# Kernel optimization log

Hardware: AMD Instinct MI355X
Metric: run time of the kernel (lower is better)

The kernel has to match this reference:

```python
import jax, jax.numpy as jnp
import numpy as np

B, S, D, H = 2, 2048, 1024, 16
HD = D // H  # head dim = 64


def setup_inputs() -> dict:
    key = jax.random.key(0)
    ks = jax.random.split(key, 9)
    s_in = 1.0 / np.sqrt(D)
    s_out = 1.0 / np.sqrt(HD)
    return {
        "x": jax.random.normal(ks[0], (B, S, D), jnp.float32),
        "Wq": jax.random.normal(ks[1], (D, H, HD), jnp.float32) * s_in,
        "bq": jnp.zeros((H, HD), jnp.float32),
        "Wk": jax.random.normal(ks[2], (D, H, HD), jnp.float32) * s_in,
        "bk": jnp.zeros((H, HD), jnp.float32),
        "Wv": jax.random.normal(ks[3], (D, H, HD), jnp.float32) * s_in,
        "bv": jnp.zeros((H, HD), jnp.float32),
        "Wo": jax.random.normal(ks[4], (H, HD, D), jnp.float32) * s_out,
        "bo": jnp.zeros((D,), jnp.float32),
    }


def reference(x, Wq, bq, Wk, bk, Wv, bv, Wo, bo):
    # QKV projections: [B,S,D] -> [B,S,H,HD]
    q = jnp.einsum("bsd,dhk->bshk", x, Wq) + bq
    k = jnp.einsum("bsd,dhk->bshk", x, Wk) + bk
    v = jnp.einsum("bsd,dhk->bshk", x, Wv) + bv

    # scaled dot-product attention (matches nnx.dot_product_attention)
    scale = jnp.asarray(1.0 / np.sqrt(HD), q.dtype)
    scores = jnp.einsum("bqhk,bshk->bhqs", q * scale, k)  # [B,H,S,S]
    attn = jax.nn.softmax(scores, axis=-1)
    y = jnp.einsum("bhqs,bshk->bqhk", attn, v)  # [B,S,H,HD]

    # exclusive post-processing: subtract projection onto L2-normalized v
    eps = jnp.asarray(1e-12, v.dtype)
    v_norm = v * jax.lax.rsqrt(jnp.sum(jnp.square(v), axis=-1, keepdims=True) + eps)
    y = y - jnp.sum(y * v_norm, axis=-1, keepdims=True) * v_norm

    # output projection: [B,S,H,HD] -> [B,S,D]
    out = jnp.einsum("bshk,hkd->bsd", y, Wo) + bo
    return out  # dropout is identity (deterministic=True)
```

## Files before the change

kernel.cpp:

```cpp
#include <hip/hip_runtime.h>

#define BB 2
#define SS 2048
#define DD 1024
#define HH 16
#define HDD 64

typedef __attribute__((ext_vector_type(4))) float f32x4;
typedef __attribute__((ext_vector_type(8))) short short8;
typedef __attribute__((ext_vector_type(4))) short short4v;

__device__ __forceinline__ short f2bf(float f) {
    union { float f; unsigned u; } a; a.f = f;
    unsigned r = a.u + 0x7fffu + ((a.u >> 16) & 1u);
    return (short)(r >> 16);
}
__device__ __forceinline__ float bf2f(short s) {
    union { unsigned u; float f; } a; a.u = ((unsigned)(unsigned short)s) << 16;
    return a.f;
}
__device__ __forceinline__ float fast_exp2(float x) {
    float r;
    asm("v_exp_f32 %0, %1\n\ts_nop 0" : "=v"(r) : "v"(x));
    return r;
}
__device__ __forceinline__ unsigned cvt_pk_bf16(float lo, float hi) {
    unsigned r;
    asm("v_cvt_pk_bf16_f32 %0, %1, %2" : "=v"(r) : "v"(lo), "v"(hi));
    return r;
}
__device__ __forceinline__ float fmax3(float a, float b, float c) {
    float r;
    asm("v_max3_f32 %0, %1, %2, %3" : "=v"(r) : "v"(a), "v"(b), "v"(c));
    return r;
}

#define GLD16(gp, lp) __builtin_amdgcn_global_load_lds( \
    (const __attribute__((address_space(1))) void*)(gp), \
    (__attribute__((address_space(3))) void*)(lp), 16, 0, 0)

__global__ __launch_bounds__(256) void conv_all(
    const float* __restrict__ x,
    const float* __restrict__ Wq, const float* __restrict__ Wk,
    const float* __restrict__ Wv, const float* __restrict__ Wo,
    short* __restrict__ xb, short* __restrict__ Wt, short* __restrict__ Wot,
    float qscale)
{
    const int z = blockIdx.z;
    if (z == 4) {
        const int id = blockIdx.x * 16 + blockIdx.y;
        const size_t base = (size_t)id * 16384 + threadIdx.x * 8;
        #pragma unroll
        for (int it = 0; it < 8; ++it) {
            const size_t i = base + (size_t)it * 2048;
            f32x4 a = *(const f32x4*)(x + i);
            f32x4 b = *(const f32x4*)(x + i + 4);
            short8 o;
            #pragma unroll
            for (int j = 0; j < 4; j++) { o[j] = f2bf(a[j]); o[j + 4] = f2bf(b[j]); }
            *(short8*)(xb + i) = o;
        }
        return;
    }
    __shared__ float t[64][65];
    const float* src = (z == 0) ? Wq : (z == 1) ? Wk : (z == 2) ? Wv : Wo;
    short* dst = (z < 3) ? (Wt + (size_t)z * 1048576) : Wot;
    const float scale = (z == 0) ? qscale : 1.f;

    const int tid = threadIdx.x;
    const int c = tid & 63, rg = tid >> 6;
    const int bi = blockIdx.x * 64, bj = blockIdx.y * 64;
    #pragma unroll
    for (int i = 0; i < 16; i++)
        t[rg * 16 + i][c] = src[(size_t)(bi + rg * 16 + i) * 1024 + bj + c];
    __syncthreads();
    #pragma unroll
    for (int i = 0; i < 16; i++)
        dst[(size_t)(bj + rg * 16 + i) * 1024 + bi + c] = f2bf(scale * t[c][rg * 16 + i]);
}

template<int KIND>
__global__ __launch_bounds__(256, 2) void gemm_mfma(
    const short* __restrict__ A, const short* __restrict__ Bt,
    const float* __restrict__ b0, const float* __restrict__ b1,
    const float* __restrict__ b2, float qscale,
    short* __restrict__ oQ, short* __restrict__ oK, short* __restrict__ oV,
    float* __restrict__ oF)
{
    __shared__ short lds[32768];
    const int tid = threadIdx.x;
    const int lane = tid & 63;
    const int ln15 = lane & 15, g = lane >> 4;
    const int swl = ln15 & 7;
    const int wid = tid >> 6;
    const int wm = wid >> 1, wn = wid & 1;
    const int bm = blockIdx.x * 128;
    const int bn = blockIdx.y * 128;
    const bool vpath = (KIND == 0) && (blockIdx.y >= 16);

    f32x4 acc[4][4];
    #pragma unroll
    for (int i = 0; i < 4; i++)
        #pragma unroll
        for (int j = 0; j < 4; j++) acc[i][j] = (f32x4){0.f, 0.f, 0.f, 0.f};

    const int sr = lane >> 3, cs = lane & 7;
    const int sc8 = (cs ^ sr) << 3;
    const int rb = wid * 8;
    const short* Ak = A;
    const short* Bk = Bt;
    int aoff[4], boff[4], adst[4];
    #pragma unroll
    for (int j = 0; j < 4; j++) {
        aoff[j] = (bm + rb + j * 32 + sr) * 1024 + sc8;
        boff[j] = (bn + rb + j * 32 + sr) * 1024 + sc8;
        adst[j] = (rb + j * 32) * 64;
    }

    auto stage = [&](int BUF) {
        #pragma unroll
        for (int j = 0; j < 4; j++) {
            GLD16(Ak + aoff[j], &lds[BUF * 16384 + adst[j]]);
            GLD16(Bk + boff[j], &lds[BUF * 16384 + 8192 + adst[j]]);
        }
        Ak += 64; Bk += 64;
    };

    const char* ldsc = (const char*)lds;
    int aB[2], bB[2];
    #pragma unroll
    for (int kk = 0; kk < 2; kk++) {
        aB[kk] = (wm * 64 + ln15) * 128 + ((((kk << 2) | g) ^ swl) << 4);
        bB[kk] = 16384 + (wn * 64 + ln15) * 128 + ((((kk << 2) | g) ^ swl) << 4);
    }

    auto tilec = [&](int BUF) {
        #pragma unroll
        for (int kk = 0; kk < 2; kk++) {
            short8 af[4], bf[4];
            #pragma unroll
            for (int f = 0; f < 4; f++) {
                af[f] = *(const short8*)(ldsc + BUF * 32768 + aB[kk] + f * 2048);
                bf[f] = *(const short8*)(ldsc + BUF * 32768 + bB[kk] + f * 2048);
            }
            if (!vpath) {
                #pragma unroll
                for (int fm = 0; fm < 4; fm++)
                    #pragma unroll
                    for (int fn = 0; fn < 4; fn++)
                        acc[fm][fn] = __builtin_amdgcn_mfma_f32_16x16x32_bf16(
                            bf[fn], af[fm], acc[fm][fn], 0, 0, 0);
            } else {
                #pragma unroll
                for (int fm = 0; fm < 4; fm++)
                    #pragma unroll
                    for (int fn = 0; fn < 4; fn++)
                        acc[fm][fn] = __builtin_amdgcn_mfma_f32_16x16x32_bf16(
                            af[fm], bf[fn], acc[fm][fn], 0, 0, 0);
            }
        }
    };

    stage(0);
    asm volatile("s_waitcnt vmcnt(0)" ::: "memory");
    __builtin_amdgcn_s_barrier();

    #pragma unroll 1
    for (int i = 0; i < 7; ++i) {
        stage(1);
        tilec(0);
        asm volatile("s_waitcnt vmcnt(0) lgkmcnt(0)" ::: "memory");
        __builtin_amdgcn_s_barrier();
        stage(0);
        tilec(1);
        asm volatile("s_waitcnt vmcnt(0) lgkmcnt(0)" ::: "memory");
        __builtin_amdgcn_s_barrier();
    }
    stage(1);
    tilec(0);
    asm volatile("s_waitcnt vmcnt(0) lgkmcnt(0)" ::: "memory");
    __builtin_amdgcn_s_barrier();
    tilec(1);

    const int n_base = bn + wn * 64;

    if constexpr (KIND == 1) {
        #pragma unroll
        for (int fn = 0; fn < 4; fn++) {
            const int n0 = n_base + fn * 16 + 4 * g;
            const f32x4 b4 = *(const f32x4*)(b0 + n0);
            #pragma unroll
            for (int fm = 0; fm < 4; fm++) {
                const int t = bm + wm * 64 + fm * 16 + ln15;
                f32x4 o = acc[fm][fn] + b4;
                *(f32x4*)(oF + (size_t)t * 1024 + n0) = o;
            }
        }
    } else if (!vpath) {
        const bool isq = (n_base < 1024);
        short* dst = isq ? oQ : oK;
        const float* bp = isq ? b0 : b1;
        const float scl = isq ? qscale : 1.f;
        #pragma unroll
        for (int fn = 0; fn < 4; fn++) {
            const int n0 = n_base + fn * 16 + 4 * g;
            const int nl = n0 & 1023;
            f32x4 b4 = *(const f32x4*)(bp + nl);
            b4 *= scl;
            const int h = nl >> 6, d = nl & 63;
            #pragma unroll
            for (int fm = 0; fm < 4; fm++) {
                const int t = bm + wm * 64 + fm * 16 + ln15;
                const int b = t >> 11, s = t & 2047;
                short4v pk = { f2bf(acc[fm][fn][0] + b4[0]), f2bf(acc[fm][fn][1] + b4[1]),
                               f2bf(acc[fm][fn][2] + b4[2]), f2bf(acc[fm][fn][3] + b4[3]) };
                *(short4v*)(dst + ((size_t)(b * HH + h) * SS + s) * HDD + d) = pk;
            }
        }
    } else {
        #pragma unroll
        for (int fn = 0; fn < 4; fn++) {
            const int nf = n_base + fn * 16 + ln15;
            const int nl = nf - 2048;
            const float bb = b2[nl];
            const int h = nl >> 6, d = nl & 63;
            #pragma unroll
            for (int fm = 0; fm < 4; fm++) {
                const int t0 = bm + wm * 64 + fm * 16 + 4 * g;
                const int b = t0 >> 11;
                const int sb = (t0 & 2047) & ~63;
                const int pos = g * 16 + (fm & 1) * 4 + ((fm >> 1) & 1) * 8;
                short4v pk = { f2bf(acc[fm][fn][0] + bb), f2bf(acc[fm][fn][1] + bb),
                               f2bf(acc[fm][fn][2] + bb), f2bf(acc[fm][fn][3] + bb) };
                *(short4v*)(oV + ((size_t)(b * HH + h) * HDD + d) * SS + sb + pos) = pk;
            }
        }
    }
}

__global__ __launch_bounds__(256, 2) void attn_mfma_kernel(
    const short* __restrict__ Qh, const short* __restrict__ Kh,
    const short* __restrict__ Vt, short* __restrict__ yb)
{
    __shared__ short lds[16384];

    const int lane = threadIdx.x & 63;
    const int wid  = threadIdx.x >> 6;
    const int ln15 = lane & 15;
    const int g    = lane >> 4;
    const int swl  = ln15 & 7;

    const int bid  = ((int)blockIdx.x & 7) * 64 + ((int)blockIdx.x >> 3);
    const int bh   = bid >> 4;
    const int qB   = (bid & 15) * 128;
    const int qW   = qB + wid * 32;

    const short* qbase = Qh + (size_t)bh * SS * HDD;
    const short* kbase = Kh + (size_t)bh * SS * HDD;
    const short* vtb   = Vt + (size_t)bh * HDD * SS;

    short8 qf[2][2];
    #pragma unroll
    for (int qg = 0; qg < 2; qg++)
        #pragma unroll
        for (int c = 0; c < 2; c++)
            qf[qg][c] = *(const short8*)(qbase +
                (size_t)(qW + qg * 16 + ln15) * HDD + c * 32 + g * 8);

    const short8 ones = { 0x3f80, 0x3f80, 0x3f80, 0x3f80,
                          0x3f80, 0x3f80, 0x3f80, 0x3f80 };

    const int sr = lane >> 3;
    const int cs = lane & 7;
    const int sc8 = (cs ^ sr) << 3;
    const int r0 = wid * 16 + sr;
    const int r1 = wid * 16 + 8 + sr;
    const short* Kk = kbase;
    const short* Vk = vtb;
    const int koff0 = r0 * 64 + sc8, koff1 = r1 * 64 + sc8;
    const int voff0 = r0 * 2048 + sc8, voff1 = r1 * 2048 + sc8;
    const int d0 = (wid * 16) * 64, d1 = (wid * 16 + 8) * 64;

    auto stage = [&](int BUF) {
        GLD16(Kk + koff0, &lds[BUF * 8192 + d0]);
        GLD16(Kk + koff1, &lds[BUF * 8192 + d1]);
        GLD16(Vk + voff0, &lds[BUF * 8192 + 4096 + d0]);
        GLD16(Vk + voff1, &lds[BUF * 8192 + 4096 + d1]);
        Kk += 4096; Vk += 64;
    };

    const char* ldsc = (const char*)lds;
    const int kA0 = ln15 * 128 + ((g ^ swl) << 4);
    const int kA1 = ln15 * 128 + (((4 + g) ^ swl) << 4);
    const int vA0 = 8192 + ln15 * 128 + (((2 * g) ^ swl) << 4);
    const int vA1 = 8192 + ln15 * 128 + (((2 * g + 1) ^ swl) << 4);

    f32x4 o[2][4], ol[2];
    #pragma unroll
    for (int qg = 0; qg < 2; qg++) {
        ol[qg] = (f32x4){0.f, 0.f, 0.f, 0.f};
        #pragma unroll
        for (int c = 0; c < 4; c++) o[qg][c] = (f32x4){0.f, 0.f, 0.f, 0.f};
    }
    float m[2] = { -1e30f, -1e30f };

    auto tilec = [&](int BUF) {
        short8 kf[4][2];
        #pragma unroll
        for (int kg = 0; kg < 4; kg++) {
            kf[kg][0] = *(const short8*)(ldsc + BUF * 16384 + kA0 + kg * 2048);
            kf[kg][1] = *(const short8*)(ldsc + BUF * 16384 + kA1 + kg * 2048);
        }
        const f32x4 z = {0.f, 0.f, 0.f, 0.f};
        f32x4 s[4][2];
        __builtin_amdgcn_s_setprio(1);
        #pragma unroll
        for (int kg = 0; kg < 4; kg++)
            #pragma unroll
            for (int qg = 0; qg < 2; qg++) {
                s[kg][qg] = __builtin_amdgcn_mfma_f32_16x16x32_bf16(
                    kf[kg][0], qf[qg][0], z, 0, 0, 0);
                s[kg][qg] = __builtin_amdgcn_mfma_f32_16x16x32_bf16(
                    kf[kg][1], qf[qg][1], s[kg][qg], 0, 0, 0);
            }
        __builtin_amdgcn_s_setprio(0);

        float pm[2];
        #pragma unroll
        for (int qg = 0; qg < 2; qg++) {
            const float t0 = fmax3(s[0][qg][0], s[0][qg][1], s[0][qg][2]);
            const float t1 = fmax3(s[0][qg][3], s[1][qg][0], s[1][qg][1]);
            const float t2 = fmax3(s[1][qg][2], s[1][qg][3], s[2][qg][0]);
            const float t3 = fmax3(s[2][qg][1], s[2][qg][2], s[2][qg][3]);
            const float t4 = fmax3(s[3][qg][0], s[3][qg][1], s[3][qg][2]);
            pm[qg] = fmaxf(fmax3(t0, t1, t2), fmax3(t3, t4, s[3][qg][3]));
        }
        if (__any((pm[0] > m[0] + 8.f) || (pm[1] > m[1] + 8.f))) {
            #pragma unroll
            for (int qg = 0; qg < 2; qg++) {
                float pmw = fmaxf(pm[qg], __shfl_xor(pm[qg], 16));
                pmw = fmaxf(pmw, __shfl_xor(pmw, 32));
                const float mn = fmaxf(m[qg], pmw);
                const float corr = fast_exp2(m[qg] - mn);
                ol[qg] *= corr;
                #pragma unroll
                for (int c = 0; c < 4; c++) o[qg][c] *= corr;
                m[qg] = mn;
            }
        }

        union { unsigned u[4]; short8 v; } P0[2], P1[2];
        #pragma unroll
        for (int qg = 0; qg < 2; qg++) {
            float p[16];
            #pragma unroll
            for (int kg = 0; kg < 4; kg++)
                #pragma unroll
                for (int r = 0; r < 4; r++)
                    p[kg * 4 + r] = fast_exp2(s[kg][qg][r] - m[qg]);
            P0[qg].u[0] = cvt_pk_bf16(p[0], p[1]);
            P0[qg].u[1] = cvt_pk_bf16(p[2], p[3]);
            P0[qg].u[2] = cvt_pk_bf16(p[4], p[5]);
            P0[qg].u[3] = cvt_pk_bf16(p[6], p[7]);
            P1[qg].u[0] = cvt_pk_bf16(p[8], p[9]);
            P1[qg].u[1] = cvt_pk_bf16(p[10], p[11]);
            P1[qg].u[2] = cvt_pk_bf16(p[12], p[13]);
            P1[qg].u[3] = cvt_pk_bf16(p[14], p[15]);
        }

        __builtin_amdgcn_s_setprio(1);
        #pragma unroll
        for (int c = 0; c < 4; c++) {
            short8 vf0 = *(const short8*)(ldsc + BUF * 16384 + vA0 + c * 2048);
            short8 vf1 = *(const short8*)(ldsc + BUF * 16384 + vA1 + c * 2048);
            #pragma unroll
            for (int qg = 0; qg < 2; qg++) {
                o[qg][c] = __builtin_amdgcn_mfma_f32_16x16x32_bf16(
                    vf0, P0[qg].v, o[qg][c], 0, 0, 0);
                o[qg][c] = __builtin_amdgcn_mfma_f32_16x16x32_bf16(
                    vf1, P1[qg].v, o[qg][c], 0, 0, 0);
            }
        }
        #pragma unroll
        for (int qg = 0; qg < 2; qg++) {
            ol[qg] = __builtin_amdgcn_mfma_f32_16x16x32_bf16(ones, P0[qg].v, ol[qg], 0, 0, 0);
            ol[qg] = __builtin_amdgcn_mfma_f32_16x16x32_bf16(ones, P1[qg].v, ol[qg], 0, 0, 0);
        }
        __builtin_amdgcn_s_setprio(0);
    };

    stage(0);
    asm volatile("s_waitcnt vmcnt(0)" ::: "memory");
    __builtin_amdgcn_s_barrier();

    #pragma unroll 1
    for (int i = 0; i < 15; ++i) {
        stage(1);
        tilec(0);
        asm volatile("s_waitcnt vmcnt(0) lgkmcnt(0)" ::: "memory");
        __builtin_amdgcn_s_barrier();
        stage(0);
        tilec(1);
        asm volatile("s_waitcnt vmcnt(0) lgkmcnt(0)" ::: "memory");
        __builtin_amdgcn_s_barrier();
    }
    stage(1);
    tilec(0);
    asm volatile("s_waitcnt vmcnt(0) lgkmcnt(0)" ::: "memory");
    __builtin_amdgcn_s_barrier();
    tilec(1);

    const int b = bh >> 4, h = bh & 15;
    #pragma unroll
    for (int qg = 0; qg < 2; qg++) {
        const float inv = 1.f / ol[qg][0];
        #pragma unroll
        for (int c = 0; c < 4; c++) o[qg][c] *= inv;

        const int spos = qB + (wid >> 1) * 64 + (ln15 >> 2) * 16 + qg * 4 +
                         (wid & 1) * 8 + (ln15 & 3);
        float v4[4][4];
        float nv = 0.f, dv = 0.f;
        #pragma unroll
        for (int c = 0; c < 4; c++)
            #pragma unroll
            for (int r = 0; r < 4; r++) {
                const float vd = bf2f(vtb[(size_t)(c * 16 + 4 * g + r) * SS + spos]);
                v4[c][r] = vd;
                nv += vd * vd;
                dv += o[qg][c][r] * vd;
            }
        nv += __shfl_xor(nv, 16); nv += __shfl_xor(nv, 32);
        dv += __shfl_xor(dv, 16); dv += __shfl_xor(dv, 32);
        const float tpp = dv / (nv + 1e-12f);

        const int tok = b * SS + qW + qg * 16 + ln15;
        #pragma unroll
        for (int c = 0; c < 4; c++) {
            short4v pk = { f2bf(o[qg][c][0] - v4[c][0] * tpp),
                           f2bf(o[qg][c][1] - v4[c][1] * tpp),
                           f2bf(o[qg][c][2] - v4[c][2] * tpp),
                           f2bf(o[qg][c][3] - v4[c][3] * tpp) };
            *(short4v*)(yb + (size_t)tok * 1024 + h * 64 + c * 16 + 4 * g) = pk;
        }
    }
}

extern "C" void kernel_launch(void* const* d_in, const int* in_sizes, int n_in,
                              void* d_out, int out_size, void* d_ws, size_t ws_size,
                              hipStream_t stream)
{
    const float* x  = (const float*)d_in[0];
    const float* Wq = (const float*)d_in[1];
    const float* bq = (const float*)d_in[2];
    const float* Wk = (const float*)d_in[3];
    const float* bk = (const float*)d_in[4];
    const float* Wv = (const float*)d_in[5];
    const float* bv = (const float*)d_in[6];
    const float* Wo = (const float*)d_in[7];
    const float* bo = (const float*)d_in[8];
    float* out = (float*)d_out;

    char* w = (char*)d_ws;
    short* xb   = (short*)(w);
    short* Wt   = (short*)(w + (8ull << 20));
    short* Wot  = (short*)(w + (14ull << 20));
    short* Qh   = (short*)(w + (16ull << 20));
    short* Kh   = (short*)(w + (24ull << 20));
    short* Vt   = (short*)(w + (32ull << 20));
    short* yb   = (short*)(w + (40ull << 20));

    const float qscale = 0.125f * 1.44269504f;
    dim3 blk(256);

    conv_all<<<dim3(16, 16, 5), blk, 0, stream>>>(x, Wq, Wk, Wv, Wo,
                                                  xb, Wt, Wot, qscale);

    gemm_mfma<0><<<dim3(32, 24), blk, 0, stream>>>(xb, Wt, bq, bk, bv, qscale,
                                                   Qh, Kh, Vt, nullptr);

    attn_mfma_kernel<<<dim3(512), blk, 0, stream>>>(Qh, Kh, Vt, yb);

    gemm_mfma<1><<<dim3(32, 8), blk, 0, stream>>>(yb, Wot, bo, nullptr, nullptr, 1.f,
                                                  nullptr, nullptr, nullptr, out);
}
```

Before: 103.7 us.

## Double attention KV tile to 128 keys and shrink output-projection GEMM M tile

The attention kernel now stages 128 keys per step instead of 64, with a new swizzled V-transpose layout and twice the MFMAs per tile. This halves the number of loop iterations, barriers and online-softmax rescale checks. The output-projection GEMM uses 64-row M tiles and launches 512 blocks instead of 256, giving better CU occupancy on the small GEMM. The costs are doubled attention LDS use and higher register pressure from the larger score arrays, which may hurt occupancy.

```diff
diff --git a/kernel.cpp b/kernel.cpp
--- a/kernel.cpp
+++ b/kernel.cpp
@@ -87,42 +87,51 @@
     short* __restrict__ oQ, short* __restrict__ oK, short* __restrict__ oV,
     float* __restrict__ oF)
 {
-    __shared__ short lds[32768];
+    constexpr int BM = (KIND == 0) ? 128 : 64;
+    constexpr int FM = BM / 32;
+    constexpr int ASH = BM * 64;
+    constexpr int BUFSTR = ASH + 8192;
+
+    __shared__ short lds[2 * BUFSTR];
     const int tid = threadIdx.x;
     const int lane = tid & 63;
     const int ln15 = lane & 15, g = lane >> 4;
     const int swl = ln15 & 7;
     const int wid = tid >> 6;
     const int wm = wid >> 1, wn = wid & 1;
-    const int bm = blockIdx.x * 128;
+    const int bm = blockIdx.x * BM;
     const int bn = blockIdx.y * 128;
     const bool vpath = (KIND == 0) && (blockIdx.y >= 16);
 
-    f32x4 acc[4][4];
-    #pragma unroll
-    for (int i = 0; i < 4; i++)
+    f32x4 acc[FM][4];
+    #pragma unroll
+    for (int i = 0; i < FM; i++)
         #pragma unroll
         for (int j = 0; j < 4; j++) acc[i][j] = (f32x4){0.f, 0.f, 0.f, 0.f};
 
     const int sr = lane >> 3, cs = lane & 7;
     const int sc8 = (cs ^ sr) << 3;
-    const int rb = wid * 8;
     const short* Ak = A;
     const short* Bk = Bt;
-    int aoff[4], boff[4], adst[4];
+    int aoff[FM], adst[FM], boff[4], bdst[4];
+    #pragma unroll
+    for (int j = 0; j < FM; j++) {
+        aoff[j] = (bm + wid * (BM / 4) + j * 8 + sr) * 1024 + sc8;
+        adst[j] = (wid * (BM / 4) + j * 8) * 64;
+    }
     #pragma unroll
     for (int j = 0; j < 4; j++) {
-        aoff[j] = (bm + rb + j * 32 + sr) * 1024 + sc8;
-        boff[j] = (bn + rb + j * 32 + sr) * 1024 + sc8;
-        adst[j] = (rb + j * 32) * 64;
+        boff[j] = (bn + wid * 32 + j * 8 + sr) * 1024 + sc8;
+        bdst[j] = ASH + (wid * 32 + j * 8) * 64;
     }
 
     auto stage = [&](int BUF) {
         #pragma unroll
-        for (int j = 0; j < 4; j++) {
-            GLD16(Ak + aoff[j], &lds[BUF * 16384 + adst[j]]);
-            GLD16(Bk + boff[j], &lds[BUF * 16384 + 8192 + adst[j]]);
-        }
+        for (int j = 0; j < FM; j++)
+            GLD16(Ak + aoff[j], &lds[BUF * BUFSTR + adst[j]]);
+        #pragma unroll
+        for (int j = 0; j < 4; j++)
+            GLD16(Bk + boff[j], &lds[BUF * BUFSTR + bdst[j]]);
         Ak += 64; Bk += 64;
     };
 
@@ -130,29 +139,30 @@
     int aB[2], bB[2];
     #pragma unroll
     for (int kk = 0; kk < 2; kk++) {
-        aB[kk] = (wm * 64 + ln15) * 128 + ((((kk << 2) | g) ^ swl) << 4);
-        bB[kk] = 16384 + (wn * 64 + ln15) * 128 + ((((kk << 2) | g) ^ swl) << 4);
+        aB[kk] = (wm * (BM / 2) + ln15) * 128 + ((((kk << 2) | g) ^ swl) << 4);
+        bB[kk] = ASH * 2 + (wn * 64 + ln15) * 128 + ((((kk << 2) | g) ^ swl) << 4);
     }
 
     auto tilec = [&](int BUF) {
         #pragma unroll
         for (int kk = 0; kk < 2; kk++) {
-            short8 af[4], bf[4];
-            #pragma unroll
-            for (int f = 0; f < 4; f++) {
-                af[f] = *(const short8*)(ldsc + BUF * 32768 + aB[kk] + f * 2048);
-                bf[f] = *(const short8*)(ldsc + BUF * 32768 + bB[kk] + f * 2048);
-            }
+            short8 af[FM], bf[4];
+            #pragma unroll
+            for (int f = 0; f < FM; f++)
+                af[f] = *(const short8*)(ldsc + BUF * (BUFSTR * 2) + aB[kk] + f * 2048);
+            #pragma unroll
+            for (int f = 0; f < 4; f++)
+                bf[f] = *(const short8*)(ldsc + BUF * (BUFSTR * 2) + bB[kk] + f * 2048);
             if (!vpath) {
                 #pragma unroll
-                for (int fm = 0; fm < 4; fm++)
+                for (int fm = 0; fm < FM; fm++)
                     #pragma unroll
                     for (int fn = 0; fn < 4; fn++)
                         acc[fm][fn] = __builtin_amdgcn_mfma_f32_16x16x32_bf16(
                             bf[fn], af[fm], acc[fm][fn], 0, 0, 0);
             } else {
                 #pragma unroll
-                for (int fm = 0; fm < 4; fm++)
+                for (int fm = 0; fm < FM; fm++)
                     #pragma unroll
                     for (int fn = 0; fn < 4; fn++)
                         acc[fm][fn] = __builtin_amdgcn_mfma_f32_16x16x32_bf16(
@@ -190,8 +200,8 @@
             const int n0 = n_base + fn * 16 + 4 * g;
             const f32x4 b4 = *(const f32x4*)(b0 + n0);
             #pragma unroll
-            for (int fm = 0; fm < 4; fm++) {
-                const int t = bm + wm * 64 + fm * 16 + ln15;
+            for (int fm = 0; fm < FM; fm++) {
+                const int t = bm + wm * (BM / 2) + fm * 16 + ln15;
                 f32x4 o = acc[fm][fn] + b4;
                 *(f32x4*)(oF + (size_t)t * 1024 + n0) = o;
             }
@@ -209,8 +219,8 @@
             b4 *= scl;
             const int h = nl >> 6, d = nl & 63;
             #pragma unroll
-            for (int fm = 0; fm < 4; fm++) {
-                const int t = bm + wm * 64 + fm * 16 + ln15;
+            for (int fm = 0; fm < FM; fm++) {
+                const int t = bm + wm * (BM / 2) + fm * 16 + ln15;
                 const int b = t >> 11, s = t & 2047;
                 short4v pk = { f2bf(acc[fm][fn][0] + b4[0]), f2bf(acc[fm][fn][1] + b4[1]),
                                f2bf(acc[fm][fn][2] + b4[2]), f2bf(acc[fm][fn][3] + b4[3]) };
@@ -225,8 +235,8 @@
             const float bb = b2[nl];
             const int h = nl >> 6, d = nl & 63;
             #pragma unroll
-            for (int fm = 0; fm < 4; fm++) {
-                const int t0 = bm + wm * 64 + fm * 16 + 4 * g;
+            for (int fm = 0; fm < FM; fm++) {
+                const int t0 = bm + wm * (BM / 2) + fm * 16 + 4 * g;
                 const int b = t0 >> 11;
                 const int sb = (t0 & 2047) & ~63;
                 const int pos = g * 16 + (fm & 1) * 4 + ((fm >> 1) & 1) * 8;
@@ -242,7 +252,7 @@
     const short* __restrict__ Qh, const short* __restrict__ Kh,
     const short* __restrict__ Vt, short* __restrict__ yb)
 {
-    __shared__ short lds[16384];
+    __shared__ short lds[32768];
 
     const int lane = threadIdx.x & 63;
     const int wid  = threadIdx.x >> 6;
@@ -273,27 +283,35 @@
     const int sr = lane >> 3;
     const int cs = lane & 7;
     const int sc8 = (cs ^ sr) << 3;
-    const int r0 = wid * 16 + sr;
-    const int r1 = wid * 16 + 8 + sr;
+    const int rvl = lane >> 4;
+    const int cc = lane & 15;
     const short* Kk = kbase;
     const short* Vk = vtb;
-    const int koff0 = r0 * 64 + sc8, koff1 = r1 * 64 + sc8;
-    const int voff0 = r0 * 2048 + sc8, voff1 = r1 * 2048 + sc8;
-    const int d0 = (wid * 16) * 64, d1 = (wid * 16 + 8) * 64;
+    int koff[4], kdst[4], voff[4], vdst[4];
+    #pragma unroll
+    for (int j = 0; j < 4; j++) {
+        koff[j] = (wid * 32 + j * 8 + sr) * 64 + sc8;
+        kdst[j] = (wid * 32 + j * 8) * 64;
+        const int rv = wid * 16 + j * 4 + rvl;
+        voff[j] = rv * 2048 + ((cc ^ (rv & 7)) << 3);
+        vdst[j] = 8192 + (wid * 16 + j * 4) * 128;
+    }
 
     auto stage = [&](int BUF) {
-        GLD16(Kk + koff0, &lds[BUF * 8192 + d0]);
-        GLD16(Kk + koff1, &lds[BUF * 8192 + d1]);
-        GLD16(Vk + voff0, &lds[BUF * 8192 + 4096 + d0]);
-        GLD16(Vk + voff1, &lds[BUF * 8192 + 4096 + d1]);
-        Kk += 4096; Vk += 64;
+        #pragma unroll
+        for (int j = 0; j < 4; j++)
+            GLD16(Kk + koff[j], &lds[BUF * 16384 + kdst[j]]);
+        #pragma unroll
+        for (int j = 0; j < 4; j++)
+            GLD16(Vk + voff[j], &lds[BUF * 16384 + vdst[j]]);
+        Kk += 8192; Vk += 128;
     };
 
     const char* ldsc = (const char*)lds;
     const int kA0 = ln15 * 128 + ((g ^ swl) << 4);
     const int kA1 = ln15 * 128 + (((4 + g) ^ swl) << 4);
-    const int vA0 = 8192 + ln15 * 128 + (((2 * g) ^ swl) << 4);
-    const int vA1 = 8192 + ln15 * 128 + (((2 * g + 1) ^ swl) << 4);
+    const int vA0 = 16384 + ln15 * 256 + (((2 * g) ^ swl) << 4);
+    const int vA1 = 16384 + ln15 * 256 + (((2 * g + 1) ^ swl) << 4);
 
     f32x4 o[2][4], ol[2];
     #pragma unroll
@@ -305,35 +323,42 @@
     float m[2] = { -1e30f, -1e30f };
 
     auto tilec = [&](int BUF) {
-        short8 kf[4][2];
-        #pragma unroll
-        for (int kg = 0; kg < 4; kg++) {
-            kf[kg][0] = *(const short8*)(ldsc + BUF * 16384 + kA0 + kg * 2048);
-            kf[kg][1] = *(const short8*)(ldsc + BUF * 16384 + kA1 + kg * 2048);
-        }
+        const char* base = ldsc + BUF * 32768;
+        f32x4 s[8][2];
         const f32x4 z = {0.f, 0.f, 0.f, 0.f};
-        f32x4 s[4][2];
         __builtin_amdgcn_s_setprio(1);
         #pragma unroll
-        for (int kg = 0; kg < 4; kg++)
+        for (int kg = 0; kg < 8; kg++) {
+            const short8 k0 = *(const short8*)(base + kA0 + kg * 2048);
+            const short8 k1 = *(const short8*)(base + kA1 + kg * 2048);
             #pragma unroll
             for (int qg = 0; qg < 2; qg++) {
                 s[kg][qg] = __builtin_amdgcn_mfma_f32_16x16x32_bf16(
-                    kf[kg][0], qf[qg][0], z, 0, 0, 0);
+                    k0, qf[qg][0], z, 0, 0, 0);
                 s[kg][qg] = __builtin_amdgcn_mfma_f32_16x16x32_bf16(
-                    kf[kg][1], qf[qg][1], s[kg][qg], 0, 0, 0);
-            }
+                    k1, qf[qg][1], s[kg][qg], 0, 0, 0);
+            }
+        }
         __builtin_amdgcn_s_setprio(0);
 
         float pm[2];
         #pragma unroll
         for (int qg = 0; qg < 2; qg++) {
-            const float t0 = fmax3(s[0][qg][0], s[0][qg][1], s[0][qg][2]);
-            const float t1 = fmax3(s[0][qg][3], s[1][qg][0], s[1][qg][1]);
-            const float t2 = fmax3(s[1][qg][2], s[1][qg][3], s[2][qg][0]);
-            const float t3 = fmax3(s[2][qg][1], s[2][qg][2], s[2][qg][3]);
-            const float t4 = fmax3(s[3][qg][0], s[3][qg][1], s[3][qg][2]);
-            pm[qg] = fmaxf(fmax3(t0, t1, t2), fmax3(t3, t4, s[3][qg][3]));
+            float t0 = fmax3(s[0][qg][0], s[0][qg][1], s[0][qg][2]);
+            float t1 = fmax3(s[0][qg][3], s[1][qg][0], s[1][qg][1]);
+            float t2 = fmax3(s[1][qg][2], s[1][qg][3], s[2][qg][0]);
+            float t3 = fmax3(s[2][qg][1], s[2][qg][2], s[2][qg][3]);
+            float t4 = fmax3(s[3][qg][0], s[3][qg][1], s[3][qg][2]);
+            float t5 = fmax3(s[3][qg][3], s[4][qg][0], s[4][qg][1]);
+            float t6 = fmax3(s[4][qg][2], s[4][qg][3], s[5][qg][0]);
+            float t7 = fmax3(s[5][qg][1], s[5][qg][2], s[5][qg][3]);
+            float t8 = fmax3(s[6][qg][0], s[6][qg][1], s[6][qg][2]);
+            float t9 = fmax3(s[6][qg][3], s[7][qg][0], s[7][qg][1]);
+            float ta = fmax3(s[7][qg][2], s[7][qg][3], t0);
+            float tb = fmax3(t1, t2, t3);
+            float tc = fmax3(t4, t5, t6);
+            float td = fmax3(t7, t8, t9);
+            pm[qg] = fmax3(fmaxf(ta, tb), tc, td);
         }
         if (__any((pm[0] > m[0] + 8.f) || (pm[1] > m[1] + 8.f))) {
             #pragma unroll
@@ -349,42 +374,58 @@
             }
         }
 
-        union { unsigned u[4]; short8 v; } P0[2], P1[2];
+        union { unsigned u[4]; short8 v; } PA0[2], PA1[2], PB0[2], PB1[2];
         #pragma unroll
         for (int qg = 0; qg < 2; qg++) {
-            float p[16];
-            #pragma unroll
-            for (int kg = 0; kg < 4; kg++)
+            float p[32];
+            #pragma unroll
+            for (int kg = 0; kg < 8; kg++)
                 #pragma unroll
                 for (int r = 0; r < 4; r++)
                     p[kg * 4 + r] = fast_exp2(s[kg][qg][r] - m[qg]);
-            P0[qg].u[0] = cvt_pk_bf16(p[0], p[1]);
-            P0[qg].u[1] = cvt_pk_bf16(p[2], p[3]);
-            P0[qg].u[2] = cvt_pk_bf16(p[4], p[5]);
-            P0[qg].u[3] = cvt_pk_bf16(p[6], p[7]);
-            P1[qg].u[0] = cvt_pk_bf16(p[8], p[9]);
-            P1[qg].u[1] = cvt_pk_bf16(p[10], p[11]);
-            P1[qg].u[2] = cvt_pk_bf16(p[12], p[13]);
-            P1[qg].u[3] = cvt_pk_bf16(p[14], p[15]);
+            PA0[qg].u[0] = cvt_pk_bf16(p[0], p[1]);
+            PA0[qg].u[1] = cvt_pk_bf16(p[2], p[3]);
+            PA0[qg].u[2] = cvt_pk_bf16(p[4], p[5]);
+            PA0[qg].u[3] = cvt_pk_bf16(p[6], p[7]);
+            PA1[qg].u[0] = cvt_pk_bf16(p[8], p[9]);
+            PA1[qg].u[1] = cvt_pk_bf16(p[10], p[11]);
+            PA1[qg].u[2] = cvt_pk_bf16(p[12], p[13]);
+            PA1[qg].u[3] = cvt_pk_bf16(p[14], p[15]);
+            PB0[qg].u[0] = cvt_pk_bf16(p[16], p[17]);
+            PB0[qg].u[1] = cvt_pk_bf16(p[18], p[19]);
+            PB0[qg].u[2] = cvt_pk_bf16(p[20], p[21]);
+            PB0[qg].u[3] = cvt_pk_bf16(p[22], p[23]);
+            PB1[qg].u[0] = cvt_pk_bf16(p[24], p[25]);
+            PB1[qg].u[1] = cvt_pk_bf16(p[26], p[27]);
+            PB1[qg].u[2] = cvt_pk_bf16(p[28], p[29]);
+            PB1[qg].u[3] = cvt_pk_bf16(p[30], p[31]);
         }
 
         __builtin_amdgcn_s_setprio(1);
         #pragma unroll
         for (int c = 0; c < 4; c++) {
-            short8 vf0 = *(const short8*)(ldsc + BUF * 16384 + vA0 + c * 2048);
-            short8 vf1 = *(const short8*)(ldsc + BUF * 16384 + vA1 + c * 2048);
+            const short8 vfA0 = *(const short8*)(base + vA0 + c * 4096);
+            const short8 vfA1 = *(const short8*)(base + vA1 + c * 4096);
+            const short8 vfB0 = *(const short8*)(base + vA0 + c * 4096 + 128);
+            const short8 vfB1 = *(const short8*)(base + vA1 + c * 4096 + 128);
             #pragma unroll
             for (int qg = 0; qg < 2; qg++) {
                 o[qg][c] = __builtin_amdgcn_mfma_f32_16x16x32_bf16(
-                    vf0, P0[qg].v, o[qg][c], 0, 0, 0);
+                    vfA0, PA0[qg].v, o[qg][c], 0, 0, 0);
                 o[qg][c] = __builtin_amdgcn_mfma_f32_16x16x32_bf16(
-                    vf1, P1[qg].v, o[qg][c], 0, 0, 0);
+                    vfA1, PA1[qg].v, o[qg][c], 0, 0, 0);
+                o[qg][c] = __builtin_amdgcn_mfma_f32_16x16x32_bf16(
+                    vfB0, PB0[qg].v, o[qg][c], 0, 0, 0);
+                o[qg][c] = __builtin_amdgcn_mfma_f32_16x16x32_bf16(
+                    vfB1, PB1[qg].v, o[qg][c], 0, 0, 0);
             }
         }
         #pragma unroll
         for (int qg = 0; qg < 2; qg++) {
-            ol[qg] = __builtin_amdgcn_mfma_f32_16x16x32_bf16(ones, P0[qg].v, ol[qg], 0, 0, 0);
-            ol[qg] = __builtin_amdgcn_mfma_f32_16x16x32_bf16(ones, P1[qg].v, ol[qg], 0, 0, 0);
+            ol[qg] = __builtin_amdgcn_mfma_f32_16x16x32_bf16(ones, PA0[qg].v, ol[qg], 0, 0, 0);
+            ol[qg] = __builtin_amdgcn_mfma_f32_16x16x32_bf16(ones, PA1[qg].v, ol[qg], 0, 0, 0);
+            ol[qg] = __builtin_amdgcn_mfma_f32_16x16x32_bf16(ones, PB0[qg].v, ol[qg], 0, 0, 0);
+            ol[qg] = __builtin_amdgcn_mfma_f32_16x16x32_bf16(ones, PB1[qg].v, ol[qg], 0, 0, 0);
         }
         __builtin_amdgcn_s_setprio(0);
     };
@@ -394,7 +435,7 @@
     __builtin_amdgcn_s_barrier();
 
     #pragma unroll 1
-    for (int i = 0; i < 15; ++i) {
+    for (int i = 0; i < 7; ++i) {
         stage(1);
         tilec(0);
         asm volatile("s_waitcnt vmcnt(0) lgkmcnt(0)" ::: "memory");
@@ -481,6 +522,6 @@
 
     attn_mfma_kernel<<<dim3(512), blk, 0, stream>>>(Qh, Kh, Vt, yb);
 
-    gemm_mfma<1><<<dim3(32, 8), blk, 0, stream>>>(yb, Wot, bo, nullptr, nullptr, 1.f,
+    gemm_mfma<1><<<dim3(64, 8), blk, 0, stream>>>(yb, Wot, bo, nullptr, nullptr, 1.f,
                                                   nullptr, nullptr, nullptr, out);
 }
```

Result: no change. 103.8 us (+0.1%).
